# Kernel tuning notes

Hardware: AMD Instinct MI355X
Metric: run time of the kernel (lower is better)

## Reference

```python
import jax, jax.numpy as jnp
import numpy as np

N_NODES = 100000
N_EDGES = 3200000
D_IN, D_HID, N_CLASSES = 128, 16, 10


def gcn_conv(x, src, dst, W, b, num_nodes):
    # PyG GCNConv: h = W x; add self-loops; symmetric deg^-1/2 normalization; scatter-sum; + bias
    h = x @ W                                        # [N, d_out]
    loops = jnp.arange(num_nodes, dtype=src.dtype)
    s = jnp.concatenate([src, loops])                # [E+N]
    d = jnp.concatenate([dst, loops])                # [E+N]
    deg = jax.ops.segment_sum(jnp.ones_like(d, dtype=h.dtype), d, num_segments=num_nodes)
    dinv = jax.lax.rsqrt(jnp.maximum(deg, 1.0))      # self-loops guarantee deg >= 1
    norm = dinv[s] * dinv[d]                         # [E+N]
    msg = h[s] * norm[:, None]                       # gather + scale
    out = jax.ops.segment_sum(msg, d, num_segments=num_nodes)
    return out + b


def setup_inputs() -> dict:
    key = jax.random.key(0)
    k1, k2, k3, k4, k5, k6 = jax.random.split(key, 6)
    x = jax.random.normal(k1, (N_NODES, D_IN), dtype=jnp.float32)
    edge_index = jax.random.randint(k2, (2, N_EDGES), 0, N_NODES, dtype=jnp.int32)
    W1 = jax.random.normal(k3, (D_IN, D_HID), dtype=jnp.float32) / np.sqrt(D_IN)
    b1 = jnp.zeros((D_HID,), dtype=jnp.float32)
    W2 = jax.random.normal(k4, (D_HID, N_CLASSES), dtype=jnp.float32) / np.sqrt(D_HID)
    b2 = jnp.zeros((N_CLASSES,), dtype=jnp.float32)
    return {"x": x, "edge_index": edge_index, "W1": W1, "b1": b1, "W2": W2, "b2": b2}


def reference(x, edge_index, W1, b1, W2, b2):
    num_nodes = x.shape[0]
    src, dst = edge_index[0], edge_index[1]
    h = jax.nn.relu(gcn_conv(x, src, dst, W1, b1, num_nodes))
    # dropout is identity in eval mode
    h = gcn_conv(h, src, dst, W2, b2, num_nodes)
    return jax.nn.log_softmax(h, axis=1)
```

## Files before the change

kernel.cpp:

```cpp
#include <hip/hip_runtime.h>
#include <hip/hip_fp16.h>
#include <math.h>

#define NNODES 100000
#define BSH 7
#define NBUCK 782
#define CAP 5120
#define EPB 8192
#define PBT 512
#define EPT 16

typedef __attribute__((ext_vector_type(8))) _Float16 f16x8;
typedef __attribute__((ext_vector_type(2))) __fp16 fp16x2;
typedef __attribute__((ext_vector_type(4))) float f32x4;

__device__ inline __half2 shfl_xor_h2(__half2 v, int m) {
    union { __half2 h; int i; } u;
    u.h = v;
    u.i = __shfl_xor(u.i, m);
    return u.h;
}

__global__ void k_zero(int* __restrict__ p, int n) {
    int t = threadIdx.x;
    if (t < n) p[t] = 0;
}

__global__ __launch_bounds__(512) void k_part(const int* __restrict__ src, const int* __restrict__ dst,
                                              int* __restrict__ bcur, unsigned int* __restrict__ part,
                                              int E) {
    __shared__ int h[NBUCK];
    __shared__ int gb[NBUCK];
    int t = threadIdx.x;
    for (int i = t; i < NBUCK; i += PBT) h[i] = 0;
    __syncthreads();
    int base = blockIdx.x * EPB;
    int n = min(EPB, E - base);
    unsigned ev[EPT];
    int bv[EPT];
#pragma unroll
    for (int p = 0; p < EPT; ++p) {
        int i = t + p * PBT;
        if (i < n) {
            int s = src[base + i], d = dst[base + i];
            bv[p] = d >> BSH;
            ev[p] = (unsigned)s | ((unsigned)(d & 127) << 17);
            atomicAdd(&h[bv[p]], 1);
        } else bv[p] = -1;
    }
    __syncthreads();
    for (int bq = t; bq < NBUCK; bq += PBT) {
        int c = h[bq];
        if (c) gb[bq] = atomicAdd(&bcur[bq], c);
        h[bq] = 0;
    }
    __syncthreads();
#pragma unroll
    for (int p = 0; p < EPT; ++p) {
        if (bv[p] >= 0) {
            int pos = atomicAdd(&h[bv[p]], 1);
            int g = gb[bv[p]] + pos;
            if (g < CAP) part[(size_t)bv[p] * CAP + g] = ev[p];
        }
    }
}

__global__ __launch_bounds__(256) void k_bfill(unsigned int* __restrict__ part,
                                               const int* __restrict__ bcur,
                                               int* __restrict__ cnt, int* __restrict__ off,
                                               float* __restrict__ dinv) {
    __shared__ int lcnt[128], lscan[128], lcur[128];
    __shared__ unsigned int lraw[CAP];
    int t = threadIdx.x;
    int b = blockIdx.x;
    int ec = min(bcur[b], CAP);
    size_t base = (size_t)b * CAP;
    if (t < 128) lcnt[t] = 0;
    __syncthreads();
    for (int i = t; i < ec; i += 256) {
        unsigned v = part[base + i];
        lraw[i] = v;
        atomicAdd(&lcnt[v >> 17], 1);
    }
    __syncthreads();
    if (t < 128) lscan[t] = lcnt[t];
    __syncthreads();
    for (int d = 1; d < 128; d <<= 1) {
        int v = (t >= d && t < 128) ? lscan[t - d] : 0;
        __syncthreads();
        if (t < 128) lscan[t] += v;
        __syncthreads();
    }
    if (t < 128) {
        int ex = lscan[t] - lcnt[t];
        lcur[t] = ex;
        int node = (b << BSH) + t;
        if (node < NNODES) {
            off[node] = (int)base + ex;
            cnt[node] = lcnt[t];
            dinv[node] = rsqrtf((float)(lcnt[t] + 1));
        }
    }
    __syncthreads();
    for (int i = t; i < ec; i += 256) {
        unsigned v = lraw[i];
        int p = atomicAdd(&lcur[v >> 17], 1);
        part[base + p] = v & 0x1FFFFu;
    }
}

__global__ __launch_bounds__(256) void k_gemm1(const float* __restrict__ x, const float* __restrict__ W1,
                                               const float* __restrict__ dinv, __half* __restrict__ h1s,
                                               int n_nodes) {
    __shared__ _Float16 sWT[16 * 136];
    int t = threadIdx.x;
    for (int i = t; i < 2048; i += 256) {
        int k = i >> 4, j = i & 15;
        sWT[j * 136 + k] = (_Float16)W1[i];
    }
    __syncthreads();
    int w = t >> 6, lane = t & 63;
    int node0 = blockIdx.x * 64 + w * 16;
    int row = lane & 15, kg = lane >> 4;
    int n = node0 + row;
    const float* xp = x + (size_t)min(n, n_nodes - 1) * 128 + kg * 8;
    const _Float16* wp = &sWT[row * 136 + kg * 8];
    f32x4 acc = {0.f, 0.f, 0.f, 0.f};
#pragma unroll
    for (int s = 0; s < 4; ++s) {
        float4 xa = *(const float4*)(xp + s * 32);
        float4 xb = *(const float4*)(xp + s * 32 + 4);
        union { f16x8 v8; fp16x2 v2[4]; } A;
        A.v2[0] = __builtin_amdgcn_cvt_pkrtz(xa.x, xa.y);
        A.v2[1] = __builtin_amdgcn_cvt_pkrtz(xa.z, xa.w);
        A.v2[2] = __builtin_amdgcn_cvt_pkrtz(xb.x, xb.y);
        A.v2[3] = __builtin_amdgcn_cvt_pkrtz(xb.z, xb.w);
        f16x8 B = *(const f16x8*)(wp + s * 32);
        acc = __builtin_amdgcn_mfma_f32_16x16x32_f16(A.v8, B, acc, 0, 0, 0);
    }
#pragma unroll
    for (int i = 0; i < 4; ++i) {
        int r = kg * 4 + i;
        int nn = node0 + r;
        if (nn < n_nodes) {
            float dn = dinv[nn];
            h1s[(size_t)nn * 16 + row] = __float2half(acc[i] * dn);
        }
    }
}

__global__ __launch_bounds__(256) void k_agg1(const __half* __restrict__ h1s, const unsigned int* __restrict__ col,
                                              const int* __restrict__ off, const int* __restrict__ cnt,
                                              const float* __restrict__ dinv, const float* __restrict__ b1,
                                              const float* __restrict__ W2, __half* __restrict__ h3s,
                                              int n_nodes) {
    __shared__ float sW2[16 * 17];
    __shared__ float sB[16];
    int t = threadIdx.x;
    {
        int k = t >> 4, jj = t & 15;
        sW2[k * 17 + jj] = (jj < 10) ? W2[k * 10 + jj] : 0.f;
    }
    if (t < 16) sB[t] = b1[t];
    __syncthreads();
    int wid = (blockIdx.x * 256 + t) >> 3;
    if (wid >= n_nodes) return;
    int lane = t & 63;
    int fg = lane & 1, sl = (lane >> 1) & 3;
    int deg = cnt[wid], o = off[wid];
    __half2 a0 = __floats2half2_rn(0.f, 0.f), a1 = a0, a2 = a0, a3 = a0;
    int e = sl;
    int s_cur = (e < deg) ? (int)col[o + e] : 0;
    while (e < deg) {
        int en = e + 4;
        int s_nxt = (en < deg) ? (int)col[o + en] : 0;
        uint4 u = *(const uint4*)(h1s + (size_t)s_cur * 16 + fg * 8);
        a0 = __hadd2(a0, *(__half2*)&u.x);
        a1 = __hadd2(a1, *(__half2*)&u.y);
        a2 = __hadd2(a2, *(__half2*)&u.z);
        a3 = __hadd2(a3, *(__half2*)&u.w);
        s_cur = s_nxt;
        e = en;
    }
#pragma unroll
    for (int m = 2; m <= 4; m <<= 1) {
        a0 = __hadd2(a0, shfl_xor_h2(a0, m));
        a1 = __hadd2(a1, shfl_xor_h2(a1, m));
        a2 = __hadd2(a2, shfl_xor_h2(a2, m));
        a3 = __hadd2(a3, shfl_xor_h2(a3, m));
    }
    {
        uint4 u = *(const uint4*)(h1s + (size_t)wid * 16 + fg * 8);
        a0 = __hadd2(a0, *(__half2*)&u.x);
        a1 = __hadd2(a1, *(__half2*)&u.y);
        a2 = __hadd2(a2, *(__half2*)&u.z);
        a3 = __hadd2(a3, *(__half2*)&u.w);
    }
    float2 f01 = __half22float2(a0), f23 = __half22float2(a1);
    float2 f45 = __half22float2(a2), f67 = __half22float2(a3);
    float f[8] = {f01.x, f01.y, f23.x, f23.y, f45.x, f45.y, f67.x, f67.y};
    float dn = dinv[wid];
    int k0 = fg * 8;
    float hv[8];
#pragma unroll
    for (int i = 0; i < 8; ++i) hv[i] = fmaxf(fmaf(dn, f[i], sB[k0 + i]), 0.f);
    float p[4];
#pragma unroll
    for (int c = 0; c < 4; ++c) {
        float acc = 0.f;
#pragma unroll
        for (int i = 0; i < 8; ++i) acc = fmaf(hv[i], sW2[(k0 + i) * 17 + sl * 4 + c], acc);
        acc += __shfl_xor(acc, 1);
        p[c] = acc * dn;
    }
    if (fg == 0) {
        __half2 w0 = __floats2half2_rn(p[0], p[1]);
        __half2 w1 = __floats2half2_rn(p[2], p[3]);
        union { __half2 h[2]; uint2 u; } pk;
        pk.h[0] = w0; pk.h[1] = w1;
        *(uint2*)(h3s + (size_t)wid * 16 + sl * 4) = pk.u;
    }
}

__global__ __launch_bounds__(256) void k_agg2(const __half* __restrict__ h3s, const unsigned int* __restrict__ col,
                                              const int* __restrict__ off, const int* __restrict__ cnt,
                                              const float* __restrict__ dinv, const float* __restrict__ b2,
                                              float* __restrict__ out, int n_nodes) {
    int t = threadIdx.x;
    int wid = (blockIdx.x * 256 + t) >> 3;
    if (wid >= n_nodes) return;
    int lane = t & 63;
    int fg = lane & 1, sl = (lane >> 1) & 3;
    int deg = cnt[wid], o = off[wid];
    __half2 a0 = __floats2half2_rn(0.f, 0.f), a1 = a0, a2 = a0, a3 = a0;
    int e = sl;
    int s_cur = (e < deg) ? (int)col[o + e] : 0;
    while (e < deg) {
        int en = e + 4;
        int s_nxt = (en < deg) ? (int)col[o + en] : 0;
        uint4 u = *(const uint4*)(h3s + (size_t)s_cur * 16 + fg * 8);
        a0 = __hadd2(a0, *(__half2*)&u.x);
        a1 = __hadd2(a1, *(__half2*)&u.y);
        a2 = __hadd2(a2, *(__half2*)&u.z);
        a3 = __hadd2(a3, *(__half2*)&u.w);
        s_cur = s_nxt;
        e = en;
    }
#pragma unroll
    for (int m = 2; m <= 4; m <<= 1) {
        a0 = __hadd2(a0, shfl_xor_h2(a0, m));
        a1 = __hadd2(a1, shfl_xor_h2(a1, m));
        a2 = __hadd2(a2, shfl_xor_h2(a2, m));
        a3 = __hadd2(a3, shfl_xor_h2(a3, m));
    }
    {
        uint4 u = *(const uint4*)(h3s + (size_t)wid * 16 + fg * 8);
        a0 = __hadd2(a0, *(__half2*)&u.x);
        a1 = __hadd2(a1, *(__half2*)&u.y);
        a2 = __hadd2(a2, *(__half2*)&u.z);
        a3 = __hadd2(a3, *(__half2*)&u.w);
    }
    float2 f01 = __half22float2(a0), f23 = __half22float2(a1);
    float2 f45 = __half22float2(a2), f67 = __half22float2(a3);
    float f[8] = {f01.x, f01.y, f23.x, f23.y, f45.x, f45.y, f67.x, f67.y};
    float dn = dinv[wid];
    float v[8];
    float mx = -1e30f;
#pragma unroll
    for (int i = 0; i < 8; ++i) {
        int idx = fg * 8 + i;
        if (idx < 10) {
            v[i] = fmaf(dn, f[i], b2[idx]);
            mx = fmaxf(mx, v[i]);
        } else v[i] = 0.f;
    }
    mx = fmaxf(mx, __shfl_xor(mx, 1));
    float se = 0.f;
#pragma unroll
    for (int i = 0; i < 8; ++i) {
        int idx = fg * 8 + i;
        if (idx < 10) se += __expf(v[i] - mx);
    }
    se += __shfl_xor(se, 1);
    float lse = mx + __logf(se);
    if (sl == 0) {
#pragma unroll
        for (int i = 0; i < 8; ++i) {
            int idx = fg * 8 + i;
            if (idx < 10) out[(size_t)wid * 10 + idx] = v[i] - lse;
        }
    }
}


extern "C" void kernel_launch(void* const* d_in, const int* in_sizes, int n_in,
                              void* d_out, int out_size, void* d_ws, size_t ws_size,
                              hipStream_t stream) {
    const float* x  = (const float*)d_in[0];
    const int*   ei = (const int*)d_in[1];
    const float* W1 = (const float*)d_in[2];
    const float* b1 = (const float*)d_in[3];
    const float* W2 = (const float*)d_in[4];
    const float* b2 = (const float*)d_in[5];
    float* out = (float*)d_out;

    const int N = in_sizes[0] / 128;
    const int E = in_sizes[1] / 2;
    const int* src = ei;
    const int* dst = ei + E;

    char* ws = (char*)d_ws;
    size_t o = 0;
    auto alloc = [&](size_t bytes) {
        size_t p = o;
        o = (o + bytes + 255) & ~(size_t)255;
        return p;
    };
    int*    bcur = (int*)(ws + alloc(1024 * 4));
    int*    cnt  = (int*)(ws + alloc((size_t)N * 4));
    int*    off  = (int*)(ws + alloc((size_t)N * 4));
    float*  dinv = (float*)(ws + alloc((size_t)N * 4));
    unsigned int* part = (unsigned int*)(ws + alloc((size_t)NBUCK * CAP * 4));
    __half* h1s  = (__half*)(ws + alloc((size_t)N * 16 * 2));
    __half* h3s  = (__half*)(ws + alloc((size_t)N * 16 * 2));

    k_zero<<<1, 1024, 0, stream>>>(bcur, 1024);

    int gp = (E + EPB - 1) / EPB;
    k_part<<<gp, PBT, 0, stream>>>(src, dst, bcur, part, E);
    k_bfill<<<NBUCK, 256, 0, stream>>>(part, bcur, cnt, off, dinv);

    int gg = (N + 63) / 64;
    k_gemm1<<<gg, 256, 0, stream>>>(x, W1, dinv, h1s, N);

    int ga = (N * 8 + 255) / 256;
    k_agg1<<<ga, 256, 0, stream>>>(h1s, part, off, cnt, dinv, b1, W2, h3s, N);
    k_agg2<<<ga, 256, 0, stream>>>(h3s, part, off, cnt, dinv, b2, out, N);
}
```

Baseline: 123.8 us.

## Fuse layer-1 GEMM into bucket build kernel and vectorize edge loads

Merges the per-node x@W1 MFMA GEMM into the bucket-fill kernel, so each 128-node bucket block also computes its nodes' scaled hidden features using dinv from shared memory. This removes one launch and the global dinv re-read. The partition kernel also loads src/dst as int2 pairs to halve load instructions. The cost is more shared memory and register pressure in the build kernel, which may lower occupancy, and the int2 path assumes E is even and aligned.

```diff
diff --git a/kernel.cpp b/kernel.cpp
--- a/kernel.cpp
+++ b/kernel.cpp
@@ -36,17 +36,26 @@
     __syncthreads();
     int base = blockIdx.x * EPB;
     int n = min(EPB, E - base);
+    const int2* src2 = (const int2*)(src + base);
+    const int2* dst2 = (const int2*)(dst + base);
     unsigned ev[EPT];
     int bv[EPT];
 #pragma unroll
-    for (int p = 0; p < EPT; ++p) {
-        int i = t + p * PBT;
-        if (i < n) {
-            int s = src[base + i], d = dst[base + i];
-            bv[p] = d >> BSH;
-            ev[p] = (unsigned)s | ((unsigned)(d & 127) << 17);
-            atomicAdd(&h[bv[p]], 1);
-        } else bv[p] = -1;
+    for (int p = 0; p < EPT / 2; ++p) {
+        int i2 = t + p * PBT;
+        if (2 * i2 < n) {
+            int2 s2 = src2[i2];
+            int2 d2 = dst2[i2];
+            bv[2 * p]     = d2.x >> BSH;
+            ev[2 * p]     = (unsigned)s2.x | ((unsigned)(d2.x & 127) << 17);
+            bv[2 * p + 1] = d2.y >> BSH;
+            ev[2 * p + 1] = (unsigned)s2.y | ((unsigned)(d2.y & 127) << 17);
+            atomicAdd(&h[bv[2 * p]], 1);
+            atomicAdd(&h[bv[2 * p + 1]], 1);
+        } else {
+            bv[2 * p] = -1;
+            bv[2 * p + 1] = -1;
+        }
     }
     __syncthreads();
     for (int bq = t; bq < NBUCK; bq += PBT) {
@@ -65,17 +74,25 @@
     }
 }
 
-__global__ __launch_bounds__(256) void k_bfill(unsigned int* __restrict__ part,
+__global__ __launch_bounds__(256) void k_build(unsigned int* __restrict__ part,
                                                const int* __restrict__ bcur,
                                                int* __restrict__ cnt, int* __restrict__ off,
-                                               float* __restrict__ dinv) {
+                                               float* __restrict__ dinv,
+                                               const float* __restrict__ x, const float* __restrict__ W1,
+                                               __half* __restrict__ h1s, int n_nodes) {
     __shared__ int lcnt[128], lscan[128], lcur[128];
+    __shared__ float sdinv[128];
+    __shared__ _Float16 sWT[16 * 136];
     __shared__ unsigned int lraw[CAP];
     int t = threadIdx.x;
     int b = blockIdx.x;
     int ec = min(bcur[b], CAP);
     size_t base = (size_t)b * CAP;
     if (t < 128) lcnt[t] = 0;
+    for (int i = t; i < 2048; i += 256) {
+        int k = i >> 4, j = i & 15;
+        sWT[j * 136 + k] = (_Float16)W1[i];
+    }
     __syncthreads();
     for (int i = t; i < ec; i += 256) {
         unsigned v = part[base + i];
@@ -95,10 +112,12 @@
         int ex = lscan[t] - lcnt[t];
         lcur[t] = ex;
         int node = (b << BSH) + t;
+        float dv = rsqrtf((float)(lcnt[t] + 1));
+        sdinv[t] = dv;
         if (node < NNODES) {
             off[node] = (int)base + ex;
             cnt[node] = lcnt[t];
-            dinv[node] = rsqrtf((float)(lcnt[t] + 1));
+            dinv[node] = dv;
         }
     }
     __syncthreads();
@@ -107,44 +126,37 @@
         int p = atomicAdd(&lcur[v >> 17], 1);
         part[base + p] = v & 0x1FFFFu;
     }
-}
-
-__global__ __launch_bounds__(256) void k_gemm1(const float* __restrict__ x, const float* __restrict__ W1,
-                                               const float* __restrict__ dinv, __half* __restrict__ h1s,
-                                               int n_nodes) {
-    __shared__ _Float16 sWT[16 * 136];
-    int t = threadIdx.x;
-    for (int i = t; i < 2048; i += 256) {
-        int k = i >> 4, j = i & 15;
-        sWT[j * 136 + k] = (_Float16)W1[i];
-    }
-    __syncthreads();
     int w = t >> 6, lane = t & 63;
-    int node0 = blockIdx.x * 64 + w * 16;
     int row = lane & 15, kg = lane >> 4;
-    int n = node0 + row;
-    const float* xp = x + (size_t)min(n, n_nodes - 1) * 128 + kg * 8;
-    const _Float16* wp = &sWT[row * 136 + kg * 8];
-    f32x4 acc = {0.f, 0.f, 0.f, 0.f};
-#pragma unroll
-    for (int s = 0; s < 4; ++s) {
-        float4 xa = *(const float4*)(xp + s * 32);
-        float4 xb = *(const float4*)(xp + s * 32 + 4);
-        union { f16x8 v8; fp16x2 v2[4]; } A;
-        A.v2[0] = __builtin_amdgcn_cvt_pkrtz(xa.x, xa.y);
-        A.v2[1] = __builtin_amdgcn_cvt_pkrtz(xa.z, xa.w);
-        A.v2[2] = __builtin_amdgcn_cvt_pkrtz(xb.x, xb.y);
-        A.v2[3] = __builtin_amdgcn_cvt_pkrtz(xb.z, xb.w);
-        f16x8 B = *(const f16x8*)(wp + s * 32);
-        acc = __builtin_amdgcn_mfma_f32_16x16x32_f16(A.v8, B, acc, 0, 0, 0);
-    }
-#pragma unroll
-    for (int i = 0; i < 4; ++i) {
-        int r = kg * 4 + i;
-        int nn = node0 + r;
-        if (nn < n_nodes) {
-            float dn = dinv[nn];
-            h1s[(size_t)nn * 16 + row] = __float2half(acc[i] * dn);
+#pragma unroll
+    for (int it = 0; it < 2; ++it) {
+        int node0 = (b << BSH) + it * 64 + w * 16;
+        if (node0 < n_nodes) {
+            int n = node0 + row;
+            const float* xp = x + (size_t)min(n, n_nodes - 1) * 128 + kg * 8;
+            const _Float16* wp = &sWT[row * 136 + kg * 8];
+            f32x4 acc = {0.f, 0.f, 0.f, 0.f};
+#pragma unroll
+            for (int s = 0; s < 4; ++s) {
+                float4 xa = *(const float4*)(xp + s * 32);
+                float4 xb = *(const float4*)(xp + s * 32 + 4);
+                union { f16x8 v8; fp16x2 v2[4]; } A;
+                A.v2[0] = __builtin_amdgcn_cvt_pkrtz(xa.x, xa.y);
+                A.v2[1] = __builtin_amdgcn_cvt_pkrtz(xa.z, xa.w);
+                A.v2[2] = __builtin_amdgcn_cvt_pkrtz(xb.x, xb.y);
+                A.v2[3] = __builtin_amdgcn_cvt_pkrtz(xb.z, xb.w);
+                f16x8 B = *(const f16x8*)(wp + s * 32);
+                acc = __builtin_amdgcn_mfma_f32_16x16x32_f16(A.v8, B, acc, 0, 0, 0);
+            }
+#pragma unroll
+            for (int i = 0; i < 4; ++i) {
+                int r = kg * 4 + i;
+                int nn = node0 + r;
+                if (nn < n_nodes) {
+                    float dn = sdinv[it * 64 + w * 16 + r];
+                    h1s[(size_t)nn * 16 + row] = __float2half(acc[i] * dn);
+                }
+            }
         }
     }
 }
@@ -328,10 +340,7 @@
 
     int gp = (E + EPB - 1) / EPB;
     k_part<<<gp, PBT, 0, stream>>>(src, dst, bcur, part, E);
-    k_bfill<<<NBUCK, 256, 0, stream>>>(part, bcur, cnt, off, dinv);
-
-    int gg = (N + 63) / 64;
-    k_gemm1<<<gg, 256, 0, stream>>>(x, W1, dinv, h1s, N);
+    k_build<<<NBUCK, 256, 0, stream>>>(part, bcur, cnt, off, dinv, x, W1, h1s, N);
 
     int ga = (N * 8 + 255) / 256;
     k_agg1<<<ga, 256, 0, stream>>>(h1s, part, off, cnt, dinv, b1, W2, h3s, N);
```

Result: faster. 117.7 us (-4.9%).
